# Kernel optimization log

Measured on AMD Instinct MI355X. Metric: run time of the kernel, lower is better.

## Reference

```python
import jax, jax.numpy as jnp
import numpy as np

N_NODES = 100000
N_EDGES = 1600000
D_IN = 256
N_HEADS = 4
D_OUT = 32
NEG_SLOPE = 0.2


def setup_inputs() -> dict:
    key = jax.random.key(0)
    k1, k2, k3, k4, k5, k6 = jax.random.split(key, 6)
    x = jax.random.normal(k1, (N_NODES, D_IN), dtype=jnp.float32)
    fc_w = jax.random.normal(k2, (N_HEADS * D_OUT, D_IN), dtype=jnp.float32) * (1.0 / np.sqrt(D_IN))
    attn_l = jax.random.normal(k3, (N_HEADS, D_OUT), dtype=jnp.float32) * 0.1
    attn_r = jax.random.normal(k4, (N_HEADS, D_OUT), dtype=jnp.float32) * 0.1
    src = jax.random.randint(k5, (N_EDGES,), 0, N_NODES, dtype=jnp.int64)
    dst = jax.random.randint(k6, (N_EDGES,), 0, N_NODES, dtype=jnp.int64)
    return {"x": x, "fc_w": fc_w, "attn_l": attn_l, "attn_r": attn_r, "src": src, "dst": dst}


def reference(x, fc_w, attn_l, attn_r, src, dst):
    N = x.shape[0]
    H, F = attn_l.shape
    # Linear projection: ft = fc(x) viewed as [N, H, F]
    ft = (x @ fc_w.T).reshape(N, H, F)
    # Per-node attention logits: el = <ft, a_l>, er = <ft, a_r>  -> [N, H]
    el = jnp.einsum("nhf,hf->nh", ft, attn_l)
    er = jnp.einsum("nhf,hf->nh", ft, attn_r)
    # Edge scores: e = leaky_relu(el[src] + er[dst])  -> [E, H]
    e = el[src] + er[dst]
    e = jnp.where(e > 0, e, NEG_SLOPE * e)
    # Segment (per-destination-node) softmax over incoming edges
    m = jax.ops.segment_max(e, dst, num_segments=N)  # [N, H]
    ex = jnp.exp(e - m[dst])                          # [E, H]
    denom = jax.ops.segment_sum(ex, dst, num_segments=N)  # [N, H]
    a = ex / denom[dst]                               # [E, H]
    # Weighted scatter-sum aggregation: out[n] = sum_{e: dst=n} a_e * ft[src_e]
    out = jax.ops.segment_sum(ft[src] * a[:, :, None], dst, num_segments=N)  # [N, H, F]
    return out
```

## Files before the change

kernel.cpp:

```cpp
#include <hip/hip_runtime.h>
#include <math.h>

#define N_NODES 100000
#define N_EDGES 1600000
#define D_IN 256
#define N_HEADS 4
#define D_OUT 32
#define D_HID 128
#define NEG_SLOPE 0.2f

#define BUCKET_SHIFT 8
#define BUCKET_NODES 256
#define NB ((N_NODES + BUCKET_NODES - 1) / BUCKET_NODES)
#define CAP 6144
#define TILE 2048
#define N_TILES ((N_EDGES + TILE - 1) / TILE)

typedef __attribute__((ext_vector_type(8))) short bf16x8;
typedef __attribute__((ext_vector_type(4))) float f32x4;
typedef __attribute__((ext_vector_type(4))) unsigned int u32x4;

static __device__ __forceinline__ unsigned cvt2(float lo, float hi) {
  unsigned r;
  asm("v_cvt_pk_bf16_f32 %0, %1, %2" : "=v"(r) : "v"(lo), "v"(hi));
  return r;
}
static __device__ __forceinline__ float bfu_lo(unsigned u) {
  union { unsigned u; float f; } c; c.u = u << 16; return c.f;
}
static __device__ __forceinline__ float bfu_hi(unsigned u) {
  union { unsigned u; float f; } c; c.u = u & 0xFFFF0000u; return c.f;
}

#define LDA 40
__global__ __launch_bounds__(256) void k_gemm(const float* __restrict__ x,
                                              const float* __restrict__ w,
                                              unsigned short* __restrict__ ftb) {
  __shared__ short As[128 * LDA];
  __shared__ short Bs[128 * LDA];
  int t = threadIdx.x;
  int wave = t >> 6, lane = t & 63;
  int quad = lane >> 4, l16 = lane & 15;
  int rowBase = blockIdx.x * 128;
  int wm = (wave >> 1) * 64, wn = (wave & 1) * 64;
  f32x4 acc[4][4];
  #pragma unroll
  for (int mt = 0; mt < 4; ++mt)
    #pragma unroll
    for (int nt = 0; nt < 4; ++nt) {
      acc[mt][nt][0] = 0.f; acc[mt][nt][1] = 0.f;
      acc[mt][nt][2] = 0.f; acc[mt][nt][3] = 0.f;
    }

  for (int kb = 0; kb < D_IN; kb += 32) {
    #pragma unroll
    for (int p = 0; p < 4; ++p) {
      int idx = p * 256 + t;
      int r = idx >> 3;
      int kq = (idx & 7) * 4;
      int row = rowBase + r;
      float4 v = make_float4(0.f, 0.f, 0.f, 0.f);
      if (row < N_NODES) v = *(const float4*)&x[(size_t)row * D_IN + kb + kq];
      unsigned* d = (unsigned*)&As[r * LDA + kq];
      d[0] = cvt2(v.x, v.y);
      d[1] = cvt2(v.z, v.w);
    }
    #pragma unroll
    for (int p = 0; p < 4; ++p) {
      int idx = p * 256 + t;
      int r = idx >> 3;
      int kq = (idx & 7) * 4;
      float4 v = *(const float4*)&w[(size_t)r * D_IN + kb + kq];
      unsigned* d = (unsigned*)&Bs[r * LDA + kq];
      d[0] = cvt2(v.x, v.y);
      d[1] = cvt2(v.z, v.w);
    }
    __syncthreads();
    bf16x8 af[4], bfr[4];
    #pragma unroll
    for (int mt = 0; mt < 4; ++mt)
      af[mt] = *(const bf16x8*)&As[(wm + mt * 16 + l16) * LDA + quad * 8];
    #pragma unroll
    for (int nt = 0; nt < 4; ++nt)
      bfr[nt] = *(const bf16x8*)&Bs[(wn + nt * 16 + l16) * LDA + quad * 8];
    #pragma unroll
    for (int mt = 0; mt < 4; ++mt)
      #pragma unroll
      for (int nt = 0; nt < 4; ++nt)
        acc[mt][nt] = __builtin_amdgcn_mfma_f32_16x16x32_bf16(af[mt], bfr[nt], acc[mt][nt], 0, 0, 0);
    __syncthreads();
  }
  #pragma unroll
  for (int mt = 0; mt < 4; ++mt) {
    #pragma unroll
    for (int nt = 0; nt < 4; ++nt) {
      int col = wn + nt * 16 + l16;
      #pragma unroll
      for (int r = 0; r < 4; r += 2) {
        unsigned p = cvt2(acc[mt][nt][r], acc[mt][nt][r + 1]);
        int row = rowBase + wm + mt * 16 + quad * 4 + r;
        if (row < N_NODES)
          ftb[(size_t)row * D_HID + col] = (unsigned short)p;
        if (row + 1 < N_NODES)
          ftb[(size_t)(row + 1) * D_HID + col] = (unsigned short)(p >> 16);
      }
    }
  }
}

__global__ void k_eler(const unsigned short* __restrict__ ftb,
                       const float* __restrict__ al,
                       const float* __restrict__ ar,
                       float* __restrict__ el, float* __restrict__ er) {
  int gid = blockIdx.x * blockDim.x + threadIdx.x;
  if (gid >= N_NODES * N_HEADS) return;
  int n = gid >> 2, h = gid & 3;
  const unsigned* f = (const unsigned*)&ftb[(size_t)n * D_HID + h * D_OUT];
  const float* alh = &al[h * D_OUT];
  const float* arh = &ar[h * D_OUT];
  float sl = 0.f, sr = 0.f;
  #pragma unroll
  for (int i = 0; i < 16; ++i) {
    unsigned u = f[i];
    float lo = bfu_lo(u), hi = bfu_hi(u);
    sl += lo * alh[2 * i] + hi * alh[2 * i + 1];
    sr += lo * arh[2 * i] + hi * arh[2 * i + 1];
  }
  el[gid] = sl;
  er[gid] = sr;
}

__global__ __launch_bounds__(256) void k_bucket(const int* __restrict__ src,
                                                const int* __restrict__ dst,
                                                int* __restrict__ gfill,
                                                unsigned* __restrict__ pairs) {
  __shared__ int bcnt[NB];
  __shared__ int brsv[NB];
  __shared__ int brank[NB];
  int t = threadIdx.x;
  for (int tile = blockIdx.x; tile < N_TILES; tile += gridDim.x) {
    int e0 = tile * TILE;
    int e1 = min(e0 + TILE, N_EDGES);
    for (int i = t; i < NB; i += 256) { bcnt[i] = 0; brank[i] = 0; }
    __syncthreads();
    for (int i = e0 + t; i < e1; i += 256)
      atomicAdd(&bcnt[dst[i] >> BUCKET_SHIFT], 1);
    __syncthreads();
    for (int i = t; i < NB; i += 256) {
      int c = bcnt[i];
      brsv[i] = (c > 0) ? atomicAdd(&gfill[i], c) : 0;
    }
    __syncthreads();
    for (int i = e0 + t; i < e1; i += 256) {
      int d = dst[i];
      int s = src[i];
      int b = d >> BUCKET_SHIFT;
      int r = brsv[b] + atomicAdd(&brank[b], 1);
      if (r < CAP)
        pairs[(size_t)b * CAP + r] = ((unsigned)s << 8) | (unsigned)(d & (BUCKET_NODES - 1));
    }
    __syncthreads();
  }
}

__global__ __launch_bounds__(512) void k_scanbuckets(const int* __restrict__ gfill,
                                                     int* __restrict__ bbase,
                                                     int* __restrict__ offs) {
  __shared__ int ss[512];
  int t = threadIdx.x;
  int v = (t < NB) ? gfill[t] : 0;
  ss[t] = v;
  __syncthreads();
  #pragma unroll
  for (int d = 1; d < 512; d <<= 1) {
    int u = (t >= d) ? ss[t - d] : 0;
    __syncthreads();
    ss[t] += u;
    __syncthreads();
  }
  if (t < NB) bbase[t] = (t == 0) ? 0 : ss[t - 1];
  if (t == 0) offs[N_NODES] = N_EDGES;
}

__global__ __launch_bounds__(512) void k_localsort(const unsigned* __restrict__ pairs,
                                                   const int* __restrict__ gfill,
                                                   const int* __restrict__ bbase,
                                                   int* __restrict__ offs,
                                                   int* __restrict__ ssrc) {
  __shared__ int cnt_l[256];
  __shared__ int ss[256];
  __shared__ int cur_l[256];
  int b = blockIdx.x, t = threadIdx.x;
  int E = min(gfill[b], CAP);
  int base = bbase[b];
  const unsigned* pb = &pairs[(size_t)b * CAP];
  if (t < 256) cnt_l[t] = 0;
  __syncthreads();
  for (int i = t; i < E; i += 512)
    atomicAdd(&cnt_l[pb[i] & (BUCKET_NODES - 1)], 1);
  __syncthreads();
  if (t < 256) ss[t] = cnt_l[t];
  __syncthreads();
  #pragma unroll
  for (int d = 1; d < 256; d <<= 1) {
    int u = (t < 256 && t >= d) ? ss[t - d] : 0;
    __syncthreads();
    if (t < 256) ss[t] += u;
    __syncthreads();
  }
  if (t < 256) {
    int pre = (t == 0) ? 0 : ss[t - 1];
    int node = b * BUCKET_NODES + t;
    if (node < N_NODES) offs[node] = base + pre;
    cur_l[t] = pre;
  }
  __syncthreads();
  for (int i = t; i < E; i += 512) {
    unsigned p = pb[i];
    int pos = atomicAdd(&cur_l[p & (BUCKET_NODES - 1)], 1);
    ssrc[base + pos] = (int)(p >> 8);
  }
}

__global__ __launch_bounds__(256) void k_agg(const int* __restrict__ offs,
                                             const int* __restrict__ ssrc,
                                             const unsigned short* __restrict__ ftb,
                                             const float* __restrict__ el,
                                             const float* __restrict__ er,
                                             float* __restrict__ out) {
  __shared__ int   lds_s[4][64];
  __shared__ float lds_a[4][64][4];
  int wave = threadIdx.x >> 6;
  int lane = threadIdx.x & 63;
  int n = blockIdx.x * 4 + wave;
  if (n >= N_NODES) return;
  int start = offs[n], end = offs[n + 1];
  int deg = end - start;

  if (deg <= 64) {
    float4 er4 = *(const float4*)&er[n * 4];
    bool valid = lane < deg;
    int s = valid ? ssrc[start + lane] : 0;
    float4 e4 = *(const float4*)&el[s * 4];
    float v[4] = {e4.x + er4.x, e4.y + er4.y, e4.z + er4.z, e4.w + er4.w};
    float m[4], ex[4], den[4];
    #pragma unroll
    for (int h = 0; h < 4; ++h) {
      v[h] = v[h] > 0.f ? v[h] : NEG_SLOPE * v[h];
      m[h] = valid ? v[h] : -INFINITY;
    }
    #pragma unroll
    for (int h = 0; h < 4; ++h)
      #pragma unroll
      for (int o = 32; o > 0; o >>= 1) m[h] = fmaxf(m[h], __shfl_xor(m[h], o));
    #pragma unroll
    for (int h = 0; h < 4; ++h) {
      ex[h] = valid ? __expf(v[h] - m[h]) : 0.f;
      den[h] = ex[h];
    }
    #pragma unroll
    for (int h = 0; h < 4; ++h)
      #pragma unroll
      for (int o = 32; o > 0; o >>= 1) den[h] += __shfl_xor(den[h], o);
    float4 a4 = make_float4(ex[0] / den[0], ex[1] / den[1], ex[2] / den[2], ex[3] / den[3]);
    lds_s[wave][lane] = s;
    *(float4*)&lds_a[wave][lane][0] = a4;
    __builtin_amdgcn_wave_barrier();
    int quad = lane >> 4, l4 = lane & 15;
    int head = l4 >> 2;
    const unsigned short* fb = ftb + l4 * 8;
    float acc[8] = {0.f, 0.f, 0.f, 0.f, 0.f, 0.f, 0.f, 0.f};
    for (int j = 0; j < deg; j += 4) {
      int e = j + quad;
      int sj = lds_s[wave][e];
      float a = lds_a[wave][e][head];
      u32x4 u = *(const u32x4*)&fb[(size_t)sj * D_HID];
      acc[0] += a * bfu_lo(u.x); acc[1] += a * bfu_hi(u.x);
      acc[2] += a * bfu_lo(u.y); acc[3] += a * bfu_hi(u.y);
      acc[4] += a * bfu_lo(u.z); acc[5] += a * bfu_hi(u.z);
      acc[6] += a * bfu_lo(u.w); acc[7] += a * bfu_hi(u.w);
    }
    #pragma unroll
    for (int i = 0; i < 8; ++i) {
      acc[i] += __shfl_xor(acc[i], 16);
      acc[i] += __shfl_xor(acc[i], 32);
    }
    if (quad == 0) {
      float4 o0 = make_float4(acc[0], acc[1], acc[2], acc[3]);
      float4 o1 = make_float4(acc[4], acc[5], acc[6], acc[7]);
      *(float4*)&out[(size_t)n * D_HID + l4 * 8] = o0;
      *(float4*)&out[(size_t)n * D_HID + l4 * 8 + 4] = o1;
    }
  } else {
    int f0 = lane * 2;
    int hh = lane >> 4;
    float2 acc = {0.f, 0.f};
    float4 er4 = *(const float4*)&er[n * 4];
    float erh[4] = {er4.x, er4.y, er4.z, er4.w};
    float m[4] = {-INFINITY, -INFINITY, -INFINITY, -INFINITY};
    for (int c = start; c < end; c += 64) {
      int i = c + lane;
      bool valid = i < end;
      int s = valid ? ssrc[i] : 0;
      float4 e4 = *(const float4*)&el[s * 4];
      float ee[4] = {e4.x, e4.y, e4.z, e4.w};
      #pragma unroll
      for (int h = 0; h < 4; ++h) {
        float v = ee[h] + erh[h];
        v = v > 0.f ? v : NEG_SLOPE * v;
        if (!valid) v = -INFINITY;
        m[h] = fmaxf(m[h], v);
      }
    }
    #pragma unroll
    for (int h = 0; h < 4; ++h)
      #pragma unroll
      for (int o = 32; o > 0; o >>= 1) m[h] = fmaxf(m[h], __shfl_xor(m[h], o));
    float den[4] = {0.f, 0.f, 0.f, 0.f};
    for (int c = start; c < end; c += 64) {
      int i = c + lane;
      bool valid = i < end;
      int s = valid ? ssrc[i] : 0;
      float4 e4 = *(const float4*)&el[s * 4];
      float ee[4] = {e4.x, e4.y, e4.z, e4.w};
      #pragma unroll
      for (int h = 0; h < 4; ++h) {
        float v = ee[h] + erh[h];
        v = v > 0.f ? v : NEG_SLOPE * v;
        den[h] += valid ? __expf(v - m[h]) : 0.f;
      }
    }
    #pragma unroll
    for (int h = 0; h < 4; ++h)
      #pragma unroll
      for (int o = 32; o > 0; o >>= 1) den[h] += __shfl_xor(den[h], o);
    float invd = 1.f / den[hh];
    for (int c = start; c < end; c += 64) {
      int i = c + lane;
      bool valid = i < end;
      int s = valid ? ssrc[i] : 0;
      float4 e4 = *(const float4*)&el[s * 4];
      float ee[4] = {e4.x, e4.y, e4.z, e4.w};
      float ex[4];
      #pragma unroll
      for (int h = 0; h < 4; ++h) {
        float v = ee[h] + erh[h];
        v = v > 0.f ? v : NEG_SLOPE * v;
        ex[h] = __expf(v - m[h]);
      }
      int cnt2 = min(64, end - c);
      for (int j = 0; j < cnt2; ++j) {
        int sj = __shfl(s, j);
        float a0 = __shfl(ex[0], j);
        float a1 = __shfl(ex[1], j);
        float a2 = __shfl(ex[2], j);
        float a3 = __shfl(ex[3], j);
        float ah = hh == 0 ? a0 : (hh == 1 ? a1 : (hh == 2 ? a2 : a3));
        ah *= invd;
        unsigned u = *(const unsigned*)&ftb[(size_t)sj * D_HID + f0];
        acc.x += ah * bfu_lo(u);
        acc.y += ah * bfu_hi(u);
      }
    }
    *(float2*)&out[(size_t)n * D_HID + f0] = acc;
  }
}

extern "C" void kernel_launch(void* const* d_in, const int* in_sizes, int n_in,
                              void* d_out, int out_size, void* d_ws, size_t ws_size,
                              hipStream_t stream) {
  const float* x      = (const float*)d_in[0];
  const float* fc_w   = (const float*)d_in[1];
  const float* attn_l = (const float*)d_in[2];
  const float* attn_r = (const float*)d_in[3];
  const int*   src    = (const int*)d_in[4];
  const int*   dst    = (const int*)d_in[5];
  float* out = (float*)d_out;

  char* wsp = (char*)d_ws;
  size_t off = 0;
  auto alloc = [&](size_t bytes) {
    void* p = wsp + off;
    off = (off + bytes + 255) & ~(size_t)255;
    return p;
  };
  unsigned short* ftb = (unsigned short*)alloc((size_t)N_NODES * D_HID * 2);
  float* el     = (float*)alloc((size_t)N_NODES * 4 * 4);
  float* er     = (float*)alloc((size_t)N_NODES * 4 * 4);
  int*   offs   = (int*)alloc((size_t)(N_NODES + 1) * 4);
  int*   ssrc   = (int*)alloc((size_t)N_EDGES * 4);
  int*   gfill  = (int*)alloc((size_t)NB * 4);
  int*   bbase  = (int*)alloc((size_t)NB * 4);
  unsigned* pairs = (unsigned*)alloc((size_t)NB * CAP * 4);

  hipMemsetAsync(gfill, 0, (size_t)NB * 4, stream);
  k_gemm<<<(N_NODES + 127) / 128, 256, 0, stream>>>(x, fc_w, ftb);
  k_eler<<<(N_NODES * N_HEADS + 255) / 256, 256, 0, stream>>>(ftb, attn_l, attn_r, el, er);
  k_bucket<<<N_TILES, 256, 0, stream>>>(src, dst, gfill, pairs);
  k_scanbuckets<<<1, 512, 0, stream>>>(gfill, bbase, offs);
  k_localsort<<<NB, 512, 0, stream>>>(pairs, gfill, bbase, offs, ssrc);
  k_agg<<<(N_NODES + 3) / 4, 256, 0, stream>>>(offs, ssrc, ftb, el, er, out);
}
```

Before: 344.3 us.

## Replace bucketed CSR sort with global counting sort; restructure small-degree aggregation

Replaces the two-level bucket-then-local-sort CSR construction with a direct counting sort. Per-node counts come from global atomics, followed by a block sum, a scan and per-node offsets, then an atomic scatter of src into position. This removes the intermediate pairs buffer and its fixed CAP limit, at the cost of more kernel launches and heavily contended global atomics. The small-degree aggregation path also now assigns each lane two features and walks edges four at a time, loading 4-byte words instead of 16-byte vectors. The attention weights are stored head-major so they can be read as float4.

Measured after the change: 469.6 us. 36.4% more time.

```diff
diff --git a/kernel.cpp b/kernel.cpp
--- a/kernel.cpp
+++ b/kernel.cpp
@@ -9,16 +9,10 @@
 #define D_HID 128
 #define NEG_SLOPE 0.2f
 
-#define BUCKET_SHIFT 8
-#define BUCKET_NODES 256
-#define NB ((N_NODES + BUCKET_NODES - 1) / BUCKET_NODES)
-#define CAP 6144
-#define TILE 2048
-#define N_TILES ((N_EDGES + TILE - 1) / TILE)
+#define NB ((N_NODES + 255) / 256)
 
 typedef __attribute__((ext_vector_type(8))) short bf16x8;
 typedef __attribute__((ext_vector_type(4))) float f32x4;
-typedef __attribute__((ext_vector_type(4))) unsigned int u32x4;
 
 static __device__ __forceinline__ unsigned cvt2(float lo, float hi) {
   unsigned r;
@@ -130,45 +124,31 @@
   er[gid] = sr;
 }
 
-__global__ __launch_bounds__(256) void k_bucket(const int* __restrict__ src,
-                                                const int* __restrict__ dst,
-                                                int* __restrict__ gfill,
-                                                unsigned* __restrict__ pairs) {
-  __shared__ int bcnt[NB];
-  __shared__ int brsv[NB];
-  __shared__ int brank[NB];
-  int t = threadIdx.x;
-  for (int tile = blockIdx.x; tile < N_TILES; tile += gridDim.x) {
-    int e0 = tile * TILE;
-    int e1 = min(e0 + TILE, N_EDGES);
-    for (int i = t; i < NB; i += 256) { bcnt[i] = 0; brank[i] = 0; }
-    __syncthreads();
-    for (int i = e0 + t; i < e1; i += 256)
-      atomicAdd(&bcnt[dst[i] >> BUCKET_SHIFT], 1);
-    __syncthreads();
-    for (int i = t; i < NB; i += 256) {
-      int c = bcnt[i];
-      brsv[i] = (c > 0) ? atomicAdd(&gfill[i], c) : 0;
-    }
-    __syncthreads();
-    for (int i = e0 + t; i < e1; i += 256) {
-      int d = dst[i];
-      int s = src[i];
-      int b = d >> BUCKET_SHIFT;
-      int r = brsv[b] + atomicAdd(&brank[b], 1);
-      if (r < CAP)
-        pairs[(size_t)b * CAP + r] = ((unsigned)s << 8) | (unsigned)(d & (BUCKET_NODES - 1));
-    }
-    __syncthreads();
-  }
-}
-
-__global__ __launch_bounds__(512) void k_scanbuckets(const int* __restrict__ gfill,
+__global__ __launch_bounds__(256) void k_count(const int* __restrict__ dst,
+                                               int* __restrict__ cnt) {
+  int i = blockIdx.x * 256 + threadIdx.x;
+  if (i < N_EDGES) atomicAdd(&cnt[dst[i]], 1);
+}
+
+__global__ __launch_bounds__(256) void k_blocksum(const int* __restrict__ cnt,
+                                                  int* __restrict__ bsum) {
+  __shared__ int red[4];
+  int b = blockIdx.x, t = threadIdx.x;
+  int node = b * 256 + t;
+  int v = (node < N_NODES) ? cnt[node] : 0;
+  #pragma unroll
+  for (int o = 32; o > 0; o >>= 1) v += __shfl_xor(v, o);
+  if ((t & 63) == 0) red[t >> 6] = v;
+  __syncthreads();
+  if (t == 0) bsum[b] = red[0] + red[1] + red[2] + red[3];
+}
+
+__global__ __launch_bounds__(512) void k_scanbuckets(const int* __restrict__ bsum,
                                                      int* __restrict__ bbase,
                                                      int* __restrict__ offs) {
   __shared__ int ss[512];
   int t = threadIdx.x;
-  int v = (t < NB) ? gfill[t] : 0;
+  int v = (t < NB) ? bsum[t] : 0;
   ss[t] = v;
   __syncthreads();
   #pragma unroll
@@ -182,43 +162,38 @@
   if (t == 0) offs[N_NODES] = N_EDGES;
 }
 
-__global__ __launch_bounds__(512) void k_localsort(const unsigned* __restrict__ pairs,
-                                                   const int* __restrict__ gfill,
+__global__ __launch_bounds__(256) void k_scanwrite(const int* __restrict__ cnt,
                                                    const int* __restrict__ bbase,
                                                    int* __restrict__ offs,
-                                                   int* __restrict__ ssrc) {
-  __shared__ int cnt_l[256];
+                                                   int* __restrict__ cur) {
   __shared__ int ss[256];
-  __shared__ int cur_l[256];
   int b = blockIdx.x, t = threadIdx.x;
-  int E = min(gfill[b], CAP);
-  int base = bbase[b];
-  const unsigned* pb = &pairs[(size_t)b * CAP];
-  if (t < 256) cnt_l[t] = 0;
+  int node = b * 256 + t;
+  int v = (node < N_NODES) ? cnt[node] : 0;
+  ss[t] = v;
   __syncthreads();
-  for (int i = t; i < E; i += 512)
-    atomicAdd(&cnt_l[pb[i] & (BUCKET_NODES - 1)], 1);
-  __syncthreads();
-  if (t < 256) ss[t] = cnt_l[t];
-  __syncthreads();
   #pragma unroll
   for (int d = 1; d < 256; d <<= 1) {
-    int u = (t < 256 && t >= d) ? ss[t - d] : 0;
-    __syncthreads();
-    if (t < 256) ss[t] += u;
-    __syncthreads();
-  }
-  if (t < 256) {
-    int pre = (t == 0) ? 0 : ss[t - 1];
-    int node = b * BUCKET_NODES + t;
-    if (node < N_NODES) offs[node] = base + pre;
-    cur_l[t] = pre;
-  }
-  __syncthreads();
-  for (int i = t; i < E; i += 512) {
-    unsigned p = pb[i];
-    int pos = atomicAdd(&cur_l[p & (BUCKET_NODES - 1)], 1);
-    ssrc[base + pos] = (int)(p >> 8);
+    int u = (t >= d) ? ss[t - d] : 0;
+    __syncthreads();
+    ss[t] += u;
+    __syncthreads();
+  }
+  if (node < N_NODES) {
+    int o = bbase[b] + ss[t] - v;
+    offs[node] = o;
+    cur[node] = o;
+  }
+}
+
+__global__ __launch_bounds__(256) void k_scatter(const int* __restrict__ src,
+                                                 const int* __restrict__ dst,
+                                                 int* __restrict__ cur,
+                                                 int* __restrict__ ssrc) {
+  int i = blockIdx.x * 256 + threadIdx.x;
+  if (i < N_EDGES) {
+    int pos = atomicAdd(&cur[dst[i]], 1);
+    ssrc[pos] = src[i];
   }
 }
 
@@ -229,7 +204,7 @@
                                              const float* __restrict__ er,
                                              float* __restrict__ out) {
   __shared__ int   lds_s[4][64];
-  __shared__ float lds_a[4][64][4];
+  __shared__ float lds_ah[4][4][64];
   int wave = threadIdx.x >> 6;
   int lane = threadIdx.x & 63;
   int n = blockIdx.x * 4 + wave;
@@ -262,35 +237,40 @@
     for (int h = 0; h < 4; ++h)
       #pragma unroll
       for (int o = 32; o > 0; o >>= 1) den[h] += __shfl_xor(den[h], o);
-    float4 a4 = make_float4(ex[0] / den[0], ex[1] / den[1], ex[2] / den[2], ex[3] / den[3]);
     lds_s[wave][lane] = s;
-    *(float4*)&lds_a[wave][lane][0] = a4;
+    #pragma unroll
+    for (int h = 0; h < 4; ++h)
+      lds_ah[wave][h][lane] = ex[h] / den[h];
     __builtin_amdgcn_wave_barrier();
-    int quad = lane >> 4, l4 = lane & 15;
-    int head = l4 >> 2;
-    const unsigned short* fb = ftb + l4 * 8;
-    float acc[8] = {0.f, 0.f, 0.f, 0.f, 0.f, 0.f, 0.f, 0.f};
-    for (int j = 0; j < deg; j += 4) {
-      int e = j + quad;
-      int sj = lds_s[wave][e];
-      float a = lds_a[wave][e][head];
-      u32x4 u = *(const u32x4*)&fb[(size_t)sj * D_HID];
-      acc[0] += a * bfu_lo(u.x); acc[1] += a * bfu_hi(u.x);
-      acc[2] += a * bfu_lo(u.y); acc[3] += a * bfu_hi(u.y);
-      acc[4] += a * bfu_lo(u.z); acc[5] += a * bfu_hi(u.z);
-      acc[6] += a * bfu_lo(u.w); acc[7] += a * bfu_hi(u.w);
-    }
-    #pragma unroll
-    for (int i = 0; i < 8; ++i) {
-      acc[i] += __shfl_xor(acc[i], 16);
-      acc[i] += __shfl_xor(acc[i], 32);
-    }
-    if (quad == 0) {
-      float4 o0 = make_float4(acc[0], acc[1], acc[2], acc[3]);
-      float4 o1 = make_float4(acc[4], acc[5], acc[6], acc[7]);
-      *(float4*)&out[(size_t)n * D_HID + l4 * 8] = o0;
-      *(float4*)&out[(size_t)n * D_HID + l4 * 8 + 4] = o1;
-    }
+
+    int f0 = lane * 2;
+    int hh = lane >> 4;
+    const unsigned short* fb = ftb + f0;
+    float2 acc0 = {0.f, 0.f}, acc1 = {0.f, 0.f};
+    float2 acc2 = {0.f, 0.f}, acc3 = {0.f, 0.f};
+    int j = 0;
+    for (; j + 4 <= deg; j += 4) {
+      int4   sv = *(const int4*)&lds_s[wave][j];
+      float4 av = *(const float4*)&lds_ah[wave][hh][j];
+      unsigned u0 = *(const unsigned*)&fb[(size_t)sv.x * D_HID];
+      unsigned u1 = *(const unsigned*)&fb[(size_t)sv.y * D_HID];
+      unsigned u2 = *(const unsigned*)&fb[(size_t)sv.z * D_HID];
+      unsigned u3 = *(const unsigned*)&fb[(size_t)sv.w * D_HID];
+      acc0.x += av.x * bfu_lo(u0); acc0.y += av.x * bfu_hi(u0);
+      acc1.x += av.y * bfu_lo(u1); acc1.y += av.y * bfu_hi(u1);
+      acc2.x += av.z * bfu_lo(u2); acc2.y += av.z * bfu_hi(u2);
+      acc3.x += av.w * bfu_lo(u3); acc3.y += av.w * bfu_hi(u3);
+    }
+    for (; j < deg; ++j) {
+      int sj = lds_s[wave][j];
+      float a = lds_ah[wave][hh][j];
+      unsigned u = *(const unsigned*)&fb[(size_t)sj * D_HID];
+      acc0.x += a * bfu_lo(u); acc0.y += a * bfu_hi(u);
+    }
+    float2 acc;
+    acc.x = (acc0.x + acc1.x) + (acc2.x + acc3.x);
+    acc.y = (acc0.y + acc1.y) + (acc2.y + acc3.y);
+    *(float2*)&out[(size_t)n * D_HID + f0] = acc;
   } else {
     int f0 = lane * 2;
     int hh = lane >> 4;
@@ -389,15 +369,18 @@
   float* er     = (float*)alloc((size_t)N_NODES * 4 * 4);
   int*   offs   = (int*)alloc((size_t)(N_NODES + 1) * 4);
   int*   ssrc   = (int*)alloc((size_t)N_EDGES * 4);
-  int*   gfill  = (int*)alloc((size_t)NB * 4);
+  int*   cnt    = (int*)alloc((size_t)N_NODES * 4);
+  int*   cur    = (int*)alloc((size_t)N_NODES * 4);
+  int*   bsum   = (int*)alloc((size_t)NB * 4);
   int*   bbase  = (int*)alloc((size_t)NB * 4);
-  unsigned* pairs = (unsigned*)alloc((size_t)NB * CAP * 4);
-
-  hipMemsetAsync(gfill, 0, (size_t)NB * 4, stream);
+
+  hipMemsetAsync(cnt, 0, (size_t)N_NODES * 4, stream);
   k_gemm<<<(N_NODES + 127) / 128, 256, 0, stream>>>(x, fc_w, ftb);
   k_eler<<<(N_NODES * N_HEADS + 255) / 256, 256, 0, stream>>>(ftb, attn_l, attn_r, el, er);
-  k_bucket<<<N_TILES, 256, 0, stream>>>(src, dst, gfill, pairs);
-  k_scanbuckets<<<1, 512, 0, stream>>>(gfill, bbase, offs);
-  k_localsort<<<NB, 512, 0, stream>>>(pairs, gfill, bbase, offs, ssrc);
+  k_count<<<(N_EDGES + 255) / 256, 256, 0, stream>>>(dst, cnt);
+  k_blocksum<<<NB, 256, 0, stream>>>(cnt, bsum);
+  k_scanbuckets<<<1, 512, 0, stream>>>(bsum, bbase, offs);
+  k_scanwrite<<<NB, 256, 0, stream>>>(cnt, bbase, offs, cur);
+  k_scatter<<<(N_EDGES + 255) / 256, 256, 0, stream>>>(src, dst, cur, ssrc);
   k_agg<<<(N_NODES + 3) / 4, 256, 0, stream>>>(offs, ssrc, ftb, el, er, out);
 }
```

## Restructure low-degree aggregation gathers and vectorize bucket edge loads

Applied to the files above, without the earlier changes.

In the aggregation kernel's path for nodes with degree up to 64, each wave is now split into two halves that take even and odd edges. Each lane covers four feature columns and issues four independent 8-byte gathers per iteration, reading edge indices and per-head attention weights as vectors from a head-major, padded LDS array. This is meant to put more gathers in flight and shorten the cross-lane reduction at the end. Separately, the bucketing kernel now has each thread load 8 contiguous edges with int4 loads and keep them in registers across both passes, so dst and src are no longer re-read from global memory. The trade-off is that each gather fetches 8 bytes instead of 16, so more load instructions are issued per edge.

New measurement: 324.7 us. -5.7%, faster.

```diff
diff --git a/kernel.cpp b/kernel.cpp
--- a/kernel.cpp
+++ b/kernel.cpp
@@ -14,11 +14,11 @@
 #define NB ((N_NODES + BUCKET_NODES - 1) / BUCKET_NODES)
 #define CAP 6144
 #define TILE 2048
+#define EPT 8
 #define N_TILES ((N_EDGES + TILE - 1) / TILE)
 
 typedef __attribute__((ext_vector_type(8))) short bf16x8;
 typedef __attribute__((ext_vector_type(4))) float f32x4;
-typedef __attribute__((ext_vector_type(4))) unsigned int u32x4;
 
 static __device__ __forceinline__ unsigned cvt2(float lo, float hi) {
   unsigned r;
@@ -139,25 +139,41 @@
   __shared__ int brank[NB];
   int t = threadIdx.x;
   for (int tile = blockIdx.x; tile < N_TILES; tile += gridDim.x) {
-    int e0 = tile * TILE;
-    int e1 = min(e0 + TILE, N_EDGES);
+    int e0 = tile * TILE + t * EPT;
     for (int i = t; i < NB; i += 256) { bcnt[i] = 0; brank[i] = 0; }
     __syncthreads();
-    for (int i = e0 + t; i < e1; i += 256)
-      atomicAdd(&bcnt[dst[i] >> BUCKET_SHIFT], 1);
+    int ds[EPT], ss[EPT];
+    if (e0 + EPT <= N_EDGES) {
+      *(int4*)&ds[0] = *(const int4*)&dst[e0];
+      *(int4*)&ds[4] = *(const int4*)&dst[e0 + 4];
+      *(int4*)&ss[0] = *(const int4*)&src[e0];
+      *(int4*)&ss[4] = *(const int4*)&src[e0 + 4];
+    } else {
+      #pragma unroll
+      for (int k = 0; k < EPT; ++k) {
+        int e = e0 + k;
+        ds[k] = (e < N_EDGES) ? dst[e] : -1;
+        ss[k] = (e < N_EDGES) ? src[e] : 0;
+      }
+    }
+    #pragma unroll
+    for (int k = 0; k < EPT; ++k)
+      if (ds[k] >= 0) atomicAdd(&bcnt[ds[k] >> BUCKET_SHIFT], 1);
     __syncthreads();
     for (int i = t; i < NB; i += 256) {
       int c = bcnt[i];
       brsv[i] = (c > 0) ? atomicAdd(&gfill[i], c) : 0;
     }
     __syncthreads();
-    for (int i = e0 + t; i < e1; i += 256) {
-      int d = dst[i];
-      int s = src[i];
-      int b = d >> BUCKET_SHIFT;
-      int r = brsv[b] + atomicAdd(&brank[b], 1);
-      if (r < CAP)
-        pairs[(size_t)b * CAP + r] = ((unsigned)s << 8) | (unsigned)(d & (BUCKET_NODES - 1));
+    #pragma unroll
+    for (int k = 0; k < EPT; ++k) {
+      if (ds[k] >= 0) {
+        int b = ds[k] >> BUCKET_SHIFT;
+        int r = brsv[b] + atomicAdd(&brank[b], 1);
+        if (r < CAP)
+          pairs[(size_t)b * CAP + r] =
+              ((unsigned)ss[k] << 8) | (unsigned)(ds[k] & (BUCKET_NODES - 1));
+      }
     }
     __syncthreads();
   }
@@ -222,6 +238,7 @@
   }
 }
 
+#define AHP 72
 __global__ __launch_bounds__(256) void k_agg(const int* __restrict__ offs,
                                              const int* __restrict__ ssrc,
                                              const unsigned short* __restrict__ ftb,
@@ -229,7 +246,7 @@
                                              const float* __restrict__ er,
                                              float* __restrict__ out) {
   __shared__ int   lds_s[4][64];
-  __shared__ float lds_a[4][64][4];
+  __shared__ float lds_ah[4][4][AHP];
   int wave = threadIdx.x >> 6;
   int lane = threadIdx.x & 63;
   int n = blockIdx.x * 4 + wave;
@@ -262,35 +279,44 @@
     for (int h = 0; h < 4; ++h)
       #pragma unroll
       for (int o = 32; o > 0; o >>= 1) den[h] += __shfl_xor(den[h], o);
-    float4 a4 = make_float4(ex[0] / den[0], ex[1] / den[1], ex[2] / den[2], ex[3] / den[3]);
     lds_s[wave][lane] = s;
-    *(float4*)&lds_a[wave][lane][0] = a4;
+    #pragma unroll
+    for (int h = 0; h < 4; ++h)
+      lds_ah[wave][h][lane] = ex[h] / den[h];
     __builtin_amdgcn_wave_barrier();
-    int quad = lane >> 4, l4 = lane & 15;
-    int head = l4 >> 2;
-    const unsigned short* fb = ftb + l4 * 8;
-    float acc[8] = {0.f, 0.f, 0.f, 0.f, 0.f, 0.f, 0.f, 0.f};
-    for (int j = 0; j < deg; j += 4) {
-      int e = j + quad;
-      int sj = lds_s[wave][e];
-      float a = lds_a[wave][e][head];
-      u32x4 u = *(const u32x4*)&fb[(size_t)sj * D_HID];
-      acc[0] += a * bfu_lo(u.x); acc[1] += a * bfu_hi(u.x);
-      acc[2] += a * bfu_lo(u.y); acc[3] += a * bfu_hi(u.y);
-      acc[4] += a * bfu_lo(u.z); acc[5] += a * bfu_hi(u.z);
-      acc[6] += a * bfu_lo(u.w); acc[7] += a * bfu_hi(u.w);
-    }
-    #pragma unroll
-    for (int i = 0; i < 8; ++i) {
-      acc[i] += __shfl_xor(acc[i], 16);
-      acc[i] += __shfl_xor(acc[i], 32);
-    }
-    if (quad == 0) {
-      float4 o0 = make_float4(acc[0], acc[1], acc[2], acc[3]);
-      float4 o1 = make_float4(acc[4], acc[5], acc[6], acc[7]);
-      *(float4*)&out[(size_t)n * D_HID + l4 * 8] = o0;
-      *(float4*)&out[(size_t)n * D_HID + l4 * 8 + 4] = o1;
-    }
+
+    int epar = lane >> 5;
+    int c4 = (lane & 31) * 4;
+    int hh = c4 >> 5;
+    const unsigned short* fb = ftb + c4;
+    float acc[4] = {0.f, 0.f, 0.f, 0.f};
+    for (int j = 0; j < deg; j += 8) {
+      int4   sv0 = *(const int4*)&lds_s[wave][j];
+      int4   sv1 = *(const int4*)&lds_s[wave][j + 4];
+      float4 av0 = *(const float4*)&lds_ah[wave][hh][j];
+      float4 av1 = *(const float4*)&lds_ah[wave][hh][j + 4];
+      int   sA = epar ? sv0.y : sv0.x;  float aA = epar ? av0.y : av0.x;
+      int   sB = epar ? sv0.w : sv0.z;  float aB = epar ? av0.w : av0.z;
+      int   sC = epar ? sv1.y : sv1.x;  float aC = epar ? av1.y : av1.x;
+      int   sD = epar ? sv1.w : sv1.z;  float aD = epar ? av1.w : av1.z;
+      uint2 uA = *(const uint2*)&fb[(size_t)sA * D_HID];
+      uint2 uB = *(const uint2*)&fb[(size_t)sB * D_HID];
+      uint2 uC = *(const uint2*)&fb[(size_t)sC * D_HID];
+      uint2 uD = *(const uint2*)&fb[(size_t)sD * D_HID];
+      acc[0] += aA * bfu_lo(uA.x); acc[1] += aA * bfu_hi(uA.x);
+      acc[2] += aA * bfu_lo(uA.y); acc[3] += aA * bfu_hi(uA.y);
+      acc[0] += aB * bfu_lo(uB.x); acc[1] += aB * bfu_hi(uB.x);
+      acc[2] += aB * bfu_lo(uB.y); acc[3] += aB * bfu_hi(uB.y);
+      acc[0] += aC * bfu_lo(uC.x); acc[1] += aC * bfu_hi(uC.x);
+      acc[2] += aC * bfu_lo(uC.y); acc[3] += aC * bfu_hi(uC.y);
+      acc[0] += aD * bfu_lo(uD.x); acc[1] += aD * bfu_hi(uD.x);
+      acc[2] += aD * bfu_lo(uD.y); acc[3] += aD * bfu_hi(uD.y);
+    }
+    #pragma unroll
+    for (int i = 0; i < 4; ++i) acc[i] += __shfl_xor(acc[i], 32);
+    if (epar == 0)
+      *(float4*)&out[(size_t)n * D_HID + c4] =
+          make_float4(acc[0], acc[1], acc[2], acc[3]);
   } else {
     int f0 = lane * 2;
     int hh = lane >> 4;
```
